# Optimization experiments

Measured on AMD Instinct MI355X. Metric: run time of the kernel, lower is better.

Reference implementation:

```python
import jax, jax.numpy as jnp
import numpy as np

DEPTH = 5
EPS = 1e-8


def setup_inputs() -> dict:
    key = jax.random.key(0)
    ks = jax.random.split(key, 7)
    N, E, Q = 50000, 1600000, 16
    return {
        "marg_i": jax.random.normal(ks[0], (N, Q), dtype=jnp.float32),
        "cav_ij": jax.random.uniform(ks[1], (E, Q), dtype=jnp.float32),
        "C": jax.random.uniform(ks[2], (Q, Q), dtype=jnp.float32),
        "field_i": jax.random.normal(ks[3], (N, Q), dtype=jnp.float32),
        "edge_dst": jax.random.randint(ks[4], (E,), 0, N, dtype=jnp.int32),
        "a1_src": jax.random.randint(ks[5], (E,), 0, N, dtype=jnp.int32),
        "indice_ij": jax.random.randint(ks[6], (E,), 0, E, dtype=jnp.int32),
    }


def reference(marg_i, cav_ij, C, field_i, edge_dst, a1_src, indice_ij):
    # Belief-propagation layers repeated DEPTH times.
    # B_ @ temp2  -> segment_sum of edge messages into destination nodes [N,Q]
    # A1 @ marg_i -> gather of source-node marginal per edge [E,Q]
    N = field_i.shape[0]

    def step(carry, _):
        marg, cav = carry
        temp2 = jnp.log(cav @ C + EPS)                                  # [E,Q]
        marg = jax.ops.segment_sum(temp2, edge_dst, num_segments=N) + field_i  # [N,Q]
        cav = jax.nn.softmax(marg[a1_src] - temp2[indice_ij], axis=1)  # [E,Q]
        return (marg, cav), None

    (marg, cav), _ = jax.lax.scan(step, (marg_i, cav_ij), None, length=DEPTH)
    return jax.nn.log_softmax(marg, axis=1)
```

## Files before the change

### kernel.cpp

```cpp
#include <hip/hip_runtime.h>
#include <hip/hip_fp16.h>

#define Q 16
#define EPS 1e-8f
#define DEPTH 5
#define BS 512
#define WSHIFT 9

typedef unsigned int u32;
typedef _Float16 h2 __attribute__((ext_vector_type(2)));


__device__ __forceinline__ u32 pack2(float a, float b) {
    __half2 h = __floats2half2_rn(a, b);
    return *(u32*)&h;
}
__device__ __forceinline__ float2 unpack2(u32 u) {
    __half2 h = *(__half2*)&u;
    return __half22float2(h);
}
__device__ __forceinline__ h2 mkh2(float a, float b) {
    h2 v; v[0] = (_Float16)a; v[1] = (_Float16)b; return v;
}


__global__ __launch_bounds__(256) void rank0_kernel(
    const int* __restrict__ dst, int* __restrict__ count,
    int* __restrict__ lrd, int E)
{
    int e = blockIdx.x * 256 + threadIdx.x;
    if (e < E) {
        int d = dst[e];
        int r = atomicAdd(&count[d], 1);
        lrd[e] = (int)(((u32)d << 16) | (u32)r);
    }
}

__global__ __launch_bounds__(256) void scan_partial(
    const int* __restrict__ count, int* __restrict__ partial, int N)
{
    __shared__ int sm[256];
    int i = blockIdx.x * 256 + threadIdx.x;
    sm[threadIdx.x] = (i < N) ? count[i] : 0;
    __syncthreads();
    for (int off = 128; off > 0; off >>= 1) {
        if (threadIdx.x < off) sm[threadIdx.x] += sm[threadIdx.x + off];
        __syncthreads();
    }
    if (threadIdx.x == 0) partial[blockIdx.x] = sm[0];
}

__global__ __launch_bounds__(1024) void scan_top(
    int* __restrict__ partial, int nb)
{
    __shared__ int sm[1024];
    int t = threadIdx.x;
    int v = (t < nb) ? partial[t] : 0;
    sm[t] = v;
    __syncthreads();
    for (int off = 1; off < 1024; off <<= 1) {
        int u = (t >= off) ? sm[t - off] : 0;
        __syncthreads();
        sm[t] += u;
        __syncthreads();
    }
    if (t < nb) partial[t] = sm[t] - v;
}

__global__ __launch_bounds__(256) void scan_final(
    const int* __restrict__ count, const int* __restrict__ partial,
    int* __restrict__ start, int* __restrict__ blist,
    int* __restrict__ bcount, int N)
{
    __shared__ int sm[256];
    int i = blockIdx.x * 256 + threadIdx.x;
    int v = (i < N) ? count[i] : 0;
    sm[threadIdx.x] = v;
    __syncthreads();
    for (int off = 1; off < 256; off <<= 1) {
        int u = (threadIdx.x >= off) ? sm[threadIdx.x - off] : 0;
        __syncthreads();
        sm[threadIdx.x] += u;
        __syncthreads();
    }
    int excl = sm[threadIdx.x] - v + partial[blockIdx.x];
    if (i < N) {
        start[i] = excl;
        bool need = (v == 0) || ((excl >> WSHIFT) != ((excl + v - 1) >> WSHIFT));
        if (need) {
            int p = atomicAdd(bcount, 1);
            blist[p] = i;
        }
    }
    if (i == N - 1) start[N] = excl + v;
}

__global__ __launch_bounds__(256) void scatter_meta(
    const int* __restrict__ a1_src, const int* __restrict__ indice,
    const int* __restrict__ lrd, const int* __restrict__ start,
    int2* __restrict__ meta2, int* __restrict__ m0e, int E)
{
    int e = blockIdx.x * 256 + threadIdx.x;
    if (e < E) {
        u32 dl = (u32)lrd[e];
        int p = start[dl >> 16] + (int)(dl & 0xffffu);
        int ie = indice[e];
        u32 dl2 = (u32)lrd[ie];
        int pik = start[dl2 >> 16] + (int)(dl2 & 0xffffu);
        int dstsrc = (int)((dl & 0xffff0000u) | (u32)a1_src[e]);
        meta2[p] = make_int2(pik, dstsrc);
        m0e[p] = e;
    }
}

__global__ __launch_bounds__(256) void binit(
    const int* __restrict__ blist, const int* __restrict__ bcount,
    const float* __restrict__ field, float* __restrict__ marg)
{
    int idx = blockIdx.x * 256 + threadIdx.x;
    int cnt = *bcount;
    if (idx >= cnt * 4) return;
    int n = blist[idx >> 2], part = idx & 3;
    ((float4*)(marg + (size_t)n * Q))[part] =
        ((const float4*)(field + (size_t)n * Q))[part];
}

template<int MODE>
__global__ __launch_bounds__(BS) void fused_round(
    const int2* __restrict__ meta2, const int* __restrict__ m0e,
    const float* __restrict__ C,
    const float* __restrict__ cav,
    const float* __restrict__ marg_in, const u32* __restrict__ t2_old,
    const int* __restrict__ start, const float* __restrict__ field,
    u32* __restrict__ t2_new, float* __restrict__ marg_out, int E)
{
    __shared__ __align__(16) h2 Csh[Q * 8];
    __shared__ float stage[BS * 17];
    __shared__ int s_nfirst, s_nlast;

    const int tid = threadIdx.x;
    const int blo = blockIdx.x * BS;
    const int bhi = min(blo + BS, E);
    const int j = blo + tid;
    const bool act = (j < E);

    int2 meta;
    float4 m0, m1, m2, m3;
    uint4 r0, r1;
    if (act) {
        meta = meta2[j];
        if (MODE == 0) {
            const float4* rp = (const float4*)(cav + (size_t)m0e[j] * Q);
            m0 = rp[0]; m1 = rp[1]; m2 = rp[2]; m3 = rp[3];
        } else {
            const int src = meta.y & 0xffff;
            const float4* mp = (const float4*)(marg_in + (size_t)src * Q);
            const uint4*  tp = (const uint4*)(t2_old + (size_t)meta.x * 8);
            m0 = mp[0]; m1 = mp[1]; m2 = mp[2]; m3 = mp[3];
            r0 = tp[0]; r1 = tp[1];
        }
    }

    if (tid < 128) {
        int q = tid >> 3, kk = tid & 7;
        Csh[q * 8 + kk] = mkh2(C[(2 * kk) * Q + q], C[(2 * kk + 1) * Q + q]);
    }
    if (act) {
        int mydst = (int)(((u32)meta.y) >> 16);
        if (j == blo)     s_nfirst = mydst;
        if (j == bhi - 1) s_nlast  = mydst;
    }
    __syncthreads();

    float t[Q];
    if (act) {
        h2 uh[8];
        float s, logs;
        if (MODE == 0) {
            uh[0] = mkh2(m0.x, m0.y); uh[1] = mkh2(m0.z, m0.w);
            uh[2] = mkh2(m1.x, m1.y); uh[3] = mkh2(m1.z, m1.w);
            uh[4] = mkh2(m2.x, m2.y); uh[5] = mkh2(m2.z, m2.w);
            uh[6] = mkh2(m3.x, m3.y); uh[7] = mkh2(m3.z, m3.w);
            s = 1.f; logs = 0.f;
        } else {
            float2 p0 = unpack2(r0.x), p1 = unpack2(r0.y),
                   p2 = unpack2(r0.z), p3 = unpack2(r0.w);
            float2 p4 = unpack2(r1.x), p5 = unpack2(r1.y),
                   p6 = unpack2(r1.z), p7 = unpack2(r1.w);

            float x[Q] = {m0.x - p0.x, m0.y - p0.y, m0.z - p1.x, m0.w - p1.y,
                          m1.x - p2.x, m1.y - p2.y, m1.z - p3.x, m1.w - p3.y,
                          m2.x - p4.x, m2.y - p4.y, m2.z - p5.x, m2.w - p5.y,
                          m3.x - p6.x, m3.y - p6.y, m3.z - p7.x, m3.w - p7.y};

            float mx = x[0];
#pragma unroll
            for (int q = 1; q < Q; ++q) mx = fmaxf(mx, x[q]);
            float u[Q];
            s = 0.f;
#pragma unroll
            for (int q = 0; q < Q; ++q) { u[q] = __expf(x[q] - mx); s += u[q]; }
            logs = __logf(s);
#pragma unroll
            for (int k = 0; k < 8; ++k) uh[k] = mkh2(u[2 * k], u[2 * k + 1]);
        }

        const float base = EPS * s;
#pragma unroll
        for (int q = 0; q < Q; ++q) {
            const uint4* cp = (const uint4*)&Csh[q * 8];
            h2 col[8];
            ((uint4*)col)[0] = cp[0];
            ((uint4*)col)[1] = cp[1];
            float acc = base;
#pragma unroll
            for (int kk = 0; kk < 8; ++kk)
                acc = __builtin_amdgcn_fdot2(uh[kk], col[kk], acc, false);
            t[q] = __logf(acc) - logs;
        }

        if (MODE != 2) {
            uint4 w0, w1;
            w0.x = pack2(t[0],  t[1]);  w0.y = pack2(t[2],  t[3]);
            w0.z = pack2(t[4],  t[5]);  w0.w = pack2(t[6],  t[7]);
            w1.x = pack2(t[8],  t[9]);  w1.y = pack2(t[10], t[11]);
            w1.z = pack2(t[12], t[13]); w1.w = pack2(t[14], t[15]);
            uint4* op = (uint4*)(t2_new + (size_t)j * 8);
            op[0] = w0; op[1] = w1;
        }
    } else {
#pragma unroll
        for (int q = 0; q < Q; ++q) t[q] = 0.f;
    }

#pragma unroll
    for (int q = 0; q < Q; ++q) stage[tid * 17 + q] = t[q];
    __syncthreads();

    const int nfirst = s_nfirst;
    const int ncnt = s_nlast - nfirst + 1;
    for (int k = tid; k < ncnt * Q; k += BS) {
        int ln = k >> 4, q = k & 15;
        int n = nfirst + ln;
        int slo = start[n], shi = start[n + 1];
        int lo = max(slo, blo), hi = min(shi, bhi);
        float s = 0.f;
        for (int sl = lo; sl < hi; ++sl) s += stage[(sl - blo) * 17 + q];
        if (slo >= blo && shi <= bhi)
            marg_out[(size_t)n * Q + q] = s + field[(size_t)n * Q + q];
        else
            atomicAdd(marg_out + (size_t)n * Q + q, s);
    }
}

__global__ __launch_bounds__(256) void node_out(
    const float* __restrict__ marg, float* __restrict__ out, int N)
{
    int i = blockIdx.x * 256 + threadIdx.x;
    if (i >= N) return;

    const float4* mp = (const float4*)(marg + (size_t)i * Q);
    float4 m0 = mp[0], m1 = mp[1], m2 = mp[2], m3 = mp[3];
    float x[Q] = {m0.x, m0.y, m0.z, m0.w, m1.x, m1.y, m1.z, m1.w,
                  m2.x, m2.y, m2.z, m2.w, m3.x, m3.y, m3.z, m3.w};

    float mx = x[0];
#pragma unroll
    for (int q = 1; q < Q; ++q) mx = fmaxf(mx, x[q]);
    float s = 0.f;
#pragma unroll
    for (int q = 0; q < Q; ++q) s += __expf(x[q] - mx);
    float lse = mx + __logf(s);

    float4* op = (float4*)(out + (size_t)i * Q);
    op[0] = make_float4(x[0]  - lse, x[1]  - lse, x[2]  - lse, x[3]  - lse);
    op[1] = make_float4(x[4]  - lse, x[5]  - lse, x[6]  - lse, x[7]  - lse);
    op[2] = make_float4(x[8]  - lse, x[9]  - lse, x[10] - lse, x[11] - lse);
    op[3] = make_float4(x[12] - lse, x[13] - lse, x[14] - lse, x[15] - lse);
}

extern "C" void kernel_launch(void* const* d_in, const int* in_sizes, int n_in,
                              void* d_out, int out_size, void* d_ws, size_t ws_size,
                              hipStream_t stream) {
    const float* cav_in   = (const float*)d_in[1];
    const float* C        = (const float*)d_in[2];
    const float* field_i  = (const float*)d_in[3];
    const int*   edge_dst = (const int*)d_in[4];
    const int*   a1_src   = (const int*)d_in[5];
    const int*   indice   = (const int*)d_in[6];
    float* out = (float*)d_out;

    const int E = in_sizes[4];
    const int N = in_sizes[0] / Q;

    char* ws = (char*)d_ws;
    const size_t t2_bytes   = (size_t)E * 32;
    const size_t node_bytes = (size_t)N * Q * sizeof(float);
    u32*   t2a    = (u32*)ws;                     ws += t2_bytes;
    u32*   t2b    = (u32*)ws;                     ws += t2_bytes;
    int2*  meta2  = (int2*)ws;                    ws += (size_t)E * 8;
    int*   m0e    = (int*)ws;                     ws += (size_t)E * 4;
    int*   lrd    = (int*)ws;                     ws += (size_t)E * 4;
    float* marg_a = (float*)ws;                   ws += node_bytes;
    float* marg_b = (float*)ws;                   ws += node_bytes;
    int*   count  = (int*)ws;                     ws += (size_t)N * 4;
    int*   bcount = (int*)ws;                     ws += 4;
    int*   start  = (int*)ws;                     ws += (size_t)(N + 1) * 4;
    int*   blist  = (int*)ws;                     ws += (size_t)N * 4;
    int*   partial= (int*)ws;

    const int eb = 256;
    const int eg = (E + eb - 1) / eb;
    const int fg = (E + BS - 1) / BS;
    const int ng = (N + eb - 1) / eb;

    hipMemsetAsync(count, 0, (size_t)N * 4 + 4, stream);
    rank0_kernel<<<eg, eb, 0, stream>>>(edge_dst, count, lrd, E);
    scan_partial<<<ng, eb, 0, stream>>>(count, partial, N);
    scan_top<<<1, 1024, 0, stream>>>(partial, ng);
    scan_final<<<ng, eb, 0, stream>>>(count, partial, start, blist, bcount, N);
    scatter_meta<<<eg, eb, 0, stream>>>(a1_src, indice, lrd, start, meta2, m0e, E);

    u32* t_cur = t2a;
    u32* t_nxt = t2b;
    float* m_in = marg_b;
    float* m_out = marg_a;
    const int bg = (N * 4 + eb - 1) / eb;

    for (int it = 0; it < DEPTH; ++it) {
        binit<<<bg, eb, 0, stream>>>(blist, bcount, field_i, m_out);
        if (it == 0)
            fused_round<0><<<fg, BS, 0, stream>>>(meta2, m0e, C, cav_in,
                                                  nullptr, nullptr, start, field_i,
                                                  t_cur, m_out, E);
        else if (it != DEPTH - 1)
            fused_round<1><<<fg, BS, 0, stream>>>(meta2, m0e, C, nullptr,
                                                  m_in, t_cur, start, field_i,
                                                  t_nxt, m_out, E);
        else
            fused_round<2><<<fg, BS, 0, stream>>>(meta2, m0e, C, nullptr,
                                                  m_in, t_cur, start, field_i,
                                                  nullptr, m_out, E);
        if (it != 0) { u32* tt = t_cur; t_cur = t_nxt; t_nxt = tt; }
        float* tm = m_in; m_in = m_out; m_out = tm;
    }

    node_out<<<ng, eb, 0, stream>>>(m_in, out, N);
}
```

Baseline: 615.2 us.

## Fuse first-round cav@C log into scatter kernel, drop m0e gather indirection

The first BP round's log(cav@C+eps) is now computed inside the scatter kernel, reading cav coalesced by original edge index and writing the packed half result straight into the dst-sorted slot. The first round then becomes a plain segment-sum kernel that reads t2 contiguously. This removes the m0e permutation array and the random 64-byte cav gather in round 0. The cost is a scattered 32-byte write per edge in the build kernel instead of a scattered 12-byte metadata write.

```diff
diff --git a/kernel.cpp b/kernel.cpp
--- a/kernel.cpp
+++ b/kernel.cpp
@@ -95,22 +95,65 @@
     if (i == N - 1) start[N] = excl + v;
 }
 
-__global__ __launch_bounds__(256) void scatter_meta(
+__global__ __launch_bounds__(256) void scatter_build(
     const int* __restrict__ a1_src, const int* __restrict__ indice,
     const int* __restrict__ lrd, const int* __restrict__ start,
-    int2* __restrict__ meta2, int* __restrict__ m0e, int E)
-{
-    int e = blockIdx.x * 256 + threadIdx.x;
-    if (e < E) {
-        u32 dl = (u32)lrd[e];
-        int p = start[dl >> 16] + (int)(dl & 0xffffu);
-        int ie = indice[e];
-        u32 dl2 = (u32)lrd[ie];
-        int pik = start[dl2 >> 16] + (int)(dl2 & 0xffffu);
-        int dstsrc = (int)((dl & 0xffff0000u) | (u32)a1_src[e]);
-        meta2[p] = make_int2(pik, dstsrc);
-        m0e[p] = e;
-    }
+    const float* __restrict__ cav, const float* __restrict__ C,
+    int2* __restrict__ meta2, u32* __restrict__ t2a, int E)
+{
+    __shared__ __align__(16) h2 Csh[Q * 8];
+
+    const int e = blockIdx.x * 256 + threadIdx.x;
+    const bool act = (e < E);
+
+    u32 dl = 0; int ie = 0, asrc = 0;
+    float4 c0, c1, c2, c3;
+    if (act) {
+        dl = (u32)lrd[e];
+        ie = indice[e];
+        asrc = a1_src[e];
+        const float4* rp = (const float4*)(cav + (size_t)e * Q);
+        c0 = rp[0]; c1 = rp[1]; c2 = rp[2]; c3 = rp[3];
+    }
+    if (threadIdx.x < 128) {
+        int q = threadIdx.x >> 3, kk = threadIdx.x & 7;
+        Csh[q * 8 + kk] = mkh2(C[(2 * kk) * Q + q], C[(2 * kk + 1) * Q + q]);
+    }
+    __syncthreads();
+    if (!act) return;
+
+    u32 dl2 = (u32)lrd[ie];
+    int p   = start[dl  >> 16] + (int)(dl  & 0xffffu);
+    int pik = start[dl2 >> 16] + (int)(dl2 & 0xffffu);
+    meta2[p] = make_int2(pik, (int)((dl & 0xffff0000u) | (u32)asrc));
+
+    h2 uh[8];
+    uh[0] = mkh2(c0.x, c0.y); uh[1] = mkh2(c0.z, c0.w);
+    uh[2] = mkh2(c1.x, c1.y); uh[3] = mkh2(c1.z, c1.w);
+    uh[4] = mkh2(c2.x, c2.y); uh[5] = mkh2(c2.z, c2.w);
+    uh[6] = mkh2(c3.x, c3.y); uh[7] = mkh2(c3.z, c3.w);
+
+    float t[Q];
+#pragma unroll
+    for (int q = 0; q < Q; ++q) {
+        const uint4* cp = (const uint4*)&Csh[q * 8];
+        h2 col[8];
+        ((uint4*)col)[0] = cp[0];
+        ((uint4*)col)[1] = cp[1];
+        float acc = EPS;
+#pragma unroll
+        for (int kk = 0; kk < 8; ++kk)
+            acc = __builtin_amdgcn_fdot2(uh[kk], col[kk], acc, false);
+        t[q] = __logf(acc);
+    }
+
+    uint4 w0, w1;
+    w0.x = pack2(t[0],  t[1]);  w0.y = pack2(t[2],  t[3]);
+    w0.z = pack2(t[4],  t[5]);  w0.w = pack2(t[6],  t[7]);
+    w1.x = pack2(t[8],  t[9]);  w1.y = pack2(t[10], t[11]);
+    w1.z = pack2(t[12], t[13]); w1.w = pack2(t[14], t[15]);
+    uint4* op = (uint4*)(t2a + (size_t)p * 8);
+    op[0] = w0; op[1] = w1;
 }
 
 __global__ __launch_bounds__(256) void binit(
@@ -125,16 +168,11 @@
         ((const float4*)(field + (size_t)n * Q))[part];
 }
 
-template<int MODE>
-__global__ __launch_bounds__(BS) void fused_round(
-    const int2* __restrict__ meta2, const int* __restrict__ m0e,
-    const float* __restrict__ C,
-    const float* __restrict__ cav,
-    const float* __restrict__ marg_in, const u32* __restrict__ t2_old,
+__global__ __launch_bounds__(BS) void segsum_round(
+    const int2* __restrict__ meta2, const u32* __restrict__ t2,
     const int* __restrict__ start, const float* __restrict__ field,
-    u32* __restrict__ t2_new, float* __restrict__ marg_out, int E)
-{
-    __shared__ __align__(16) h2 Csh[Q * 8];
+    float* __restrict__ marg_out, int E)
+{
     __shared__ float stage[BS * 17];
     __shared__ int s_nfirst, s_nlast;
 
@@ -145,27 +183,11 @@
     const bool act = (j < E);
 
     int2 meta;
-    float4 m0, m1, m2, m3;
     uint4 r0, r1;
     if (act) {
         meta = meta2[j];
-        if (MODE == 0) {
-            const float4* rp = (const float4*)(cav + (size_t)m0e[j] * Q);
-            m0 = rp[0]; m1 = rp[1]; m2 = rp[2]; m3 = rp[3];
-        } else {
-            const int src = meta.y & 0xffff;
-            const float4* mp = (const float4*)(marg_in + (size_t)src * Q);
-            const uint4*  tp = (const uint4*)(t2_old + (size_t)meta.x * 8);
-            m0 = mp[0]; m1 = mp[1]; m2 = mp[2]; m3 = mp[3];
-            r0 = tp[0]; r1 = tp[1];
-        }
-    }
-
-    if (tid < 128) {
-        int q = tid >> 3, kk = tid & 7;
-        Csh[q * 8 + kk] = mkh2(C[(2 * kk) * Q + q], C[(2 * kk + 1) * Q + q]);
-    }
-    if (act) {
+        const uint4* tp = (const uint4*)(t2 + (size_t)j * 8);
+        r0 = tp[0]; r1 = tp[1];
         int mydst = (int)(((u32)meta.y) >> 16);
         if (j == blo)     s_nfirst = mydst;
         if (j == bhi - 1) s_nlast  = mydst;
@@ -174,60 +196,14 @@
 
     float t[Q];
     if (act) {
-        h2 uh[8];
-        float s, logs;
-        if (MODE == 0) {
-            uh[0] = mkh2(m0.x, m0.y); uh[1] = mkh2(m0.z, m0.w);
-            uh[2] = mkh2(m1.x, m1.y); uh[3] = mkh2(m1.z, m1.w);
-            uh[4] = mkh2(m2.x, m2.y); uh[5] = mkh2(m2.z, m2.w);
-            uh[6] = mkh2(m3.x, m3.y); uh[7] = mkh2(m3.z, m3.w);
-            s = 1.f; logs = 0.f;
-        } else {
-            float2 p0 = unpack2(r0.x), p1 = unpack2(r0.y),
-                   p2 = unpack2(r0.z), p3 = unpack2(r0.w);
-            float2 p4 = unpack2(r1.x), p5 = unpack2(r1.y),
-                   p6 = unpack2(r1.z), p7 = unpack2(r1.w);
-
-            float x[Q] = {m0.x - p0.x, m0.y - p0.y, m0.z - p1.x, m0.w - p1.y,
-                          m1.x - p2.x, m1.y - p2.y, m1.z - p3.x, m1.w - p3.y,
-                          m2.x - p4.x, m2.y - p4.y, m2.z - p5.x, m2.w - p5.y,
-                          m3.x - p6.x, m3.y - p6.y, m3.z - p7.x, m3.w - p7.y};
-
-            float mx = x[0];
-#pragma unroll
-            for (int q = 1; q < Q; ++q) mx = fmaxf(mx, x[q]);
-            float u[Q];
-            s = 0.f;
-#pragma unroll
-            for (int q = 0; q < Q; ++q) { u[q] = __expf(x[q] - mx); s += u[q]; }
-            logs = __logf(s);
-#pragma unroll
-            for (int k = 0; k < 8; ++k) uh[k] = mkh2(u[2 * k], u[2 * k + 1]);
-        }
-
-        const float base = EPS * s;
-#pragma unroll
-        for (int q = 0; q < Q; ++q) {
-            const uint4* cp = (const uint4*)&Csh[q * 8];
-            h2 col[8];
-            ((uint4*)col)[0] = cp[0];
-            ((uint4*)col)[1] = cp[1];
-            float acc = base;
-#pragma unroll
-            for (int kk = 0; kk < 8; ++kk)
-                acc = __builtin_amdgcn_fdot2(uh[kk], col[kk], acc, false);
-            t[q] = __logf(acc) - logs;
-        }
-
-        if (MODE != 2) {
-            uint4 w0, w1;
-            w0.x = pack2(t[0],  t[1]);  w0.y = pack2(t[2],  t[3]);
-            w0.z = pack2(t[4],  t[5]);  w0.w = pack2(t[6],  t[7]);
-            w1.x = pack2(t[8],  t[9]);  w1.y = pack2(t[10], t[11]);
-            w1.z = pack2(t[12], t[13]); w1.w = pack2(t[14], t[15]);
-            uint4* op = (uint4*)(t2_new + (size_t)j * 8);
-            op[0] = w0; op[1] = w1;
-        }
+        float2 p0 = unpack2(r0.x), p1 = unpack2(r0.y),
+               p2 = unpack2(r0.z), p3 = unpack2(r0.w);
+        float2 p4 = unpack2(r1.x), p5 = unpack2(r1.y),
+               p6 = unpack2(r1.z), p7 = unpack2(r1.w);
+        t[0] = p0.x; t[1] = p0.y; t[2]  = p1.x; t[3]  = p1.y;
+        t[4] = p2.x; t[5] = p2.y; t[6]  = p3.x; t[7]  = p3.y;
+        t[8] = p4.x; t[9] = p4.y; t[10] = p5.x; t[11] = p5.y;
+        t[12] = p6.x; t[13] = p6.y; t[14] = p7.x; t[15] = p7.y;
     } else {
 #pragma unroll
         for (int q = 0; q < Q; ++q) t[q] = 0.f;
@@ -253,6 +229,119 @@
     }
 }
 
+template<int MODE>
+__global__ __launch_bounds__(BS) void fused_round(
+    const int2* __restrict__ meta2,
+    const float* __restrict__ C,
+    const float* __restrict__ marg_in, const u32* __restrict__ t2_old,
+    const int* __restrict__ start, const float* __restrict__ field,
+    u32* __restrict__ t2_new, float* __restrict__ marg_out, int E)
+{
+    __shared__ __align__(16) h2 Csh[Q * 8];
+    __shared__ float stage[BS * 17];
+    __shared__ int s_nfirst, s_nlast;
+
+    const int tid = threadIdx.x;
+    const int blo = blockIdx.x * BS;
+    const int bhi = min(blo + BS, E);
+    const int j = blo + tid;
+    const bool act = (j < E);
+
+    int2 meta;
+    float4 m0, m1, m2, m3;
+    uint4 r0, r1;
+    if (act) {
+        meta = meta2[j];
+        const int src = meta.y & 0xffff;
+        const float4* mp = (const float4*)(marg_in + (size_t)src * Q);
+        const uint4*  tp = (const uint4*)(t2_old + (size_t)meta.x * 8);
+        m0 = mp[0]; m1 = mp[1]; m2 = mp[2]; m3 = mp[3];
+        r0 = tp[0]; r1 = tp[1];
+    }
+
+    if (tid < 128) {
+        int q = tid >> 3, kk = tid & 7;
+        Csh[q * 8 + kk] = mkh2(C[(2 * kk) * Q + q], C[(2 * kk + 1) * Q + q]);
+    }
+    if (act) {
+        int mydst = (int)(((u32)meta.y) >> 16);
+        if (j == blo)     s_nfirst = mydst;
+        if (j == bhi - 1) s_nlast  = mydst;
+    }
+    __syncthreads();
+
+    float t[Q];
+    if (act) {
+        float2 p0 = unpack2(r0.x), p1 = unpack2(r0.y),
+               p2 = unpack2(r0.z), p3 = unpack2(r0.w);
+        float2 p4 = unpack2(r1.x), p5 = unpack2(r1.y),
+               p6 = unpack2(r1.z), p7 = unpack2(r1.w);
+
+        float x[Q] = {m0.x - p0.x, m0.y - p0.y, m0.z - p1.x, m0.w - p1.y,
+                      m1.x - p2.x, m1.y - p2.y, m1.z - p3.x, m1.w - p3.y,
+                      m2.x - p4.x, m2.y - p4.y, m2.z - p5.x, m2.w - p5.y,
+                      m3.x - p6.x, m3.y - p6.y, m3.z - p7.x, m3.w - p7.y};
+
+        float mx = x[0];
+#pragma unroll
+        for (int q = 1; q < Q; ++q) mx = fmaxf(mx, x[q]);
+        float u[Q];
+        float s = 0.f;
+#pragma unroll
+        for (int q = 0; q < Q; ++q) { u[q] = __expf(x[q] - mx); s += u[q]; }
+        float logs = __logf(s);
+        h2 uh[8];
+#pragma unroll
+        for (int k = 0; k < 8; ++k) uh[k] = mkh2(u[2 * k], u[2 * k + 1]);
+
+        const float base = EPS * s;
+#pragma unroll
+        for (int q = 0; q < Q; ++q) {
+            const uint4* cp = (const uint4*)&Csh[q * 8];
+            h2 col[8];
+            ((uint4*)col)[0] = cp[0];
+            ((uint4*)col)[1] = cp[1];
+            float acc = base;
+#pragma unroll
+            for (int kk = 0; kk < 8; ++kk)
+                acc = __builtin_amdgcn_fdot2(uh[kk], col[kk], acc, false);
+            t[q] = __logf(acc) - logs;
+        }
+
+        if (MODE != 2) {
+            uint4 w0, w1;
+            w0.x = pack2(t[0],  t[1]);  w0.y = pack2(t[2],  t[3]);
+            w0.z = pack2(t[4],  t[5]);  w0.w = pack2(t[6],  t[7]);
+            w1.x = pack2(t[8],  t[9]);  w1.y = pack2(t[10], t[11]);
+            w1.z = pack2(t[12], t[13]); w1.w = pack2(t[14], t[15]);
+            uint4* op = (uint4*)(t2_new + (size_t)j * 8);
+            op[0] = w0; op[1] = w1;
+        }
+    } else {
+#pragma unroll
+        for (int q = 0; q < Q; ++q) t[q] = 0.f;
+    }
+
+#pragma unroll
+    for (int q = 0; q < Q; ++q) stage[tid * 17 + q] = t[q];
+    __syncthreads();
+
+    const int nfirst = s_nfirst;
+    const int ncnt = s_nlast - nfirst + 1;
+    for (int k = tid; k < ncnt * Q; k += BS) {
+        int ln = k >> 4, q = k & 15;
+        int n = nfirst + ln;
+        int slo = start[n], shi = start[n + 1];
+        int lo = max(slo, blo), hi = min(shi, bhi);
+        float s = 0.f;
+        for (int sl = lo; sl < hi; ++sl) s += stage[(sl - blo) * 17 + q];
+        if (slo >= blo && shi <= bhi)
+            marg_out[(size_t)n * Q + q] = s + field[(size_t)n * Q + q];
+        else
+            atomicAdd(marg_out + (size_t)n * Q + q, s);
+    }
+}
+
 __global__ __launch_bounds__(256) void node_out(
     const float* __restrict__ marg, float* __restrict__ out, int N)
 {
@@ -299,7 +388,6 @@
     u32*   t2a    = (u32*)ws;                     ws += t2_bytes;
     u32*   t2b    = (u32*)ws;                     ws += t2_bytes;
     int2*  meta2  = (int2*)ws;                    ws += (size_t)E * 8;
-    int*   m0e    = (int*)ws;                     ws += (size_t)E * 4;
     int*   lrd    = (int*)ws;                     ws += (size_t)E * 4;
     float* marg_a = (float*)ws;                   ws += node_bytes;
     float* marg_b = (float*)ws;                   ws += node_bytes;
@@ -319,30 +407,29 @@
     scan_partial<<<ng, eb, 0, stream>>>(count, partial, N);
     scan_top<<<1, 1024, 0, stream>>>(partial, ng);
     scan_final<<<ng, eb, 0, stream>>>(count, partial, start, blist, bcount, N);
-    scatter_meta<<<eg, eb, 0, stream>>>(a1_src, indice, lrd, start, meta2, m0e, E);
+    scatter_build<<<eg, eb, 0, stream>>>(a1_src, indice, lrd, start,
+                                         cav_in, C, meta2, t2a, E);
+
+    float* m_in  = marg_b;
+    float* m_out = marg_a;
+    const int bg = (N * 4 + eb - 1) / eb;
+
+    binit<<<bg, eb, 0, stream>>>(blist, bcount, field_i, m_out);
+    segsum_round<<<fg, BS, 0, stream>>>(meta2, t2a, start, field_i, m_out, E);
+    { float* tm = m_in; m_in = m_out; m_out = tm; }
 
     u32* t_cur = t2a;
     u32* t_nxt = t2b;
-    float* m_in = marg_b;
-    float* m_out = marg_a;
-    const int bg = (N * 4 + eb - 1) / eb;
-
-    for (int it = 0; it < DEPTH; ++it) {
+    for (int it = 1; it < DEPTH; ++it) {
         binit<<<bg, eb, 0, stream>>>(blist, bcount, field_i, m_out);
-        if (it == 0)
-            fused_round<0><<<fg, BS, 0, stream>>>(meta2, m0e, C, cav_in,
-                                                  nullptr, nullptr, start, field_i,
-                                                  t_cur, m_out, E);
-        else if (it != DEPTH - 1)
-            fused_round<1><<<fg, BS, 0, stream>>>(meta2, m0e, C, nullptr,
-                                                  m_in, t_cur, start, field_i,
-                                                  t_nxt, m_out, E);
+        if (it != DEPTH - 1)
+            fused_round<1><<<fg, BS, 0, stream>>>(meta2, C, m_in, t_cur, start,
+                                                  field_i, t_nxt, m_out, E);
         else
-            fused_round<2><<<fg, BS, 0, stream>>>(meta2, m0e, C, nullptr,
-                                                  m_in, t_cur, start, field_i,
-                                                  nullptr, m_out, E);
-        if (it != 0) { u32* tt = t_cur; t_cur = t_nxt; t_nxt = tt; }
-        float* tm = m_in; m_in = m_out; m_out = tm;
+            fused_round<2><<<fg, BS, 0, stream>>>(meta2, C, m_in, t_cur, start,
+                                                  field_i, nullptr, m_out, E);
+        { u32* tt = t_cur; t_cur = t_nxt; t_nxt = tt; }
+        { float* tm = m_in; m_in = m_out; m_out = tm; }
     }
 
     node_out<<<ng, eb, 0, stream>>>(m_in, out, N);
```

New measurement: 601.4 us. 1.02x faster.
